# Kernel tuning notes

Measured on AMD Instinct MI355X. Metric: run time of the kernel, lower is better.

The kernel has to match this reference:

```python
import jax, jax.numpy as jnp
import numpy as np

B, L, D, H, NE, M = 4, 1024, 768, 12, 42, 8
OFFSET = 1
NEG = -1e9

def setup_inputs() -> dict:
    key = jax.random.key(0)
    k1, k2, k3, k4 = jax.random.split(key, 4)
    sequence_output = jax.random.normal(k1, (B, L, D), dtype=jnp.float32)
    attention = jax.random.uniform(k2, (B, H, L, L), dtype=jnp.float32)
    mention_idx = jax.random.randint(k3, (B, NE, M), 0, L - 2).astype(jnp.int32)
    mention_mask = jax.random.randint(k4, (B, NE, M), 0, 2).astype(jnp.int32)
    mention_mask = mention_mask.at[:, :, 0].set(1)  # every entity has >=1 mention
    return {"sequence_output": sequence_output, "attention": attention,
            "mention_idx": mention_idx, "mention_mask": mention_mask}

def reference(sequence_output, attention, mention_idx, mention_mask):
    b, l, d = sequence_output.shape
    h = attention.shape[1]
    idx = mention_idx + OFFSET                      # start + offset
    valid = (mention_mask > 0) & (idx < l)          # [B,NE,M], mirrors start+offset < c check
    idx = jnp.where(valid, idx, 0)

    # --- get_hrt: entity embedding = logsumexp over mentions, entity attn = mean over mentions ---
    flat = idx.reshape(b, -1)
    emb = jax.vmap(lambda s, i: s[i])(sequence_output, flat).reshape(b, NE, M, d)
    masked = jnp.where(valid[..., None], emb, NEG)
    ent_emb = jax.nn.logsumexp(masked, axis=2)      # [B,NE,D] (unused downstream, kept faithful)

    att = jax.vmap(lambda a, i: a[:, i])(attention, flat)        # [B,H,NE*M,L]
    att = att.reshape(b, h, NE, M, l)
    vmask = valid.astype(att.dtype)[:, None, :, :, None]         # [B,1,NE,M,1]
    cnt = jnp.maximum(valid.sum(axis=2), 1).astype(att.dtype)    # [B,NE]
    ent_att = (att * vmask).sum(axis=3) / cnt[:, None, :, None]  # [B,H,NE,L]

    # --- get_channel_map: ht_att = mean_h(h_att * t_att), row-normalize, contract with tokens ---
    ht_att = jnp.einsum('bhsl,bhtl->bstl', ent_att, ent_att) / h  # [B,NE,NE,L]
    ht_att = ht_att / (ht_att.sum(axis=-1, keepdims=True) + 1e-5)
    feature_map = jnp.einsum('bstl,bld->bstd', ht_att, sequence_output)  # [B,NE,NE,D]
    return feature_map
```

## Files before the change

kernel.cpp:

```cpp
#include <hip/hip_runtime.h>
#include <math.h>

#define B_    4
#define L_    1024
#define D_    768
#define H_    12
#define NE_   42
#define M_    8
#define NE2_  (NE_ * NE_)
#define NTRI_ 903
#define MPAD_ 1024
#define LC_   16
#define NCH_  (L_ / LC_)

typedef unsigned short u16;
typedef unsigned int   u32;
typedef __attribute__((ext_vector_type(2))) float f32x2;

__device__ __forceinline__ u16 f2bf(float f) {
    union { float f; u32 u; } c; c.f = f;
    u32 u = c.u;
    u32 r = (u + 0x7FFFu + ((u >> 16) & 1u)) >> 16;
    return (u16)r;
}

__global__ __launch_bounds__(128) void ent_att_kernel(
    const float* __restrict__ att, const int* __restrict__ midx,
    const int* __restrict__ mmask, float* __restrict__ ent) {
    const int h = blockIdx.x, e = blockIdx.y, b = blockIdx.z;
    const int t  = threadIdx.x;
    const int l0 = t * 8;
    const int mb = (b * NE_ + e) * M_;
    const size_t abase = ((size_t)(b * H_ + h)) * L_ * L_;

    float acc[8] = {0.f,0.f,0.f,0.f,0.f,0.f,0.f,0.f};
    int cnt = 0;
    for (int m = 0; m < M_; ++m) {
        int  im = midx[mb + m] + 1;
        bool v  = (mmask[mb + m] > 0) && (im < L_);
        if (v) {
            ++cnt;
            const float* row = att + abase + (size_t)im * L_ + l0;
            float4 x0 = *(const float4*)(row);
            float4 x1 = *(const float4*)(row + 4);
            acc[0] += x0.x; acc[1] += x0.y; acc[2] += x0.z; acc[3] += x0.w;
            acc[4] += x1.x; acc[5] += x1.y; acc[6] += x1.z; acc[7] += x1.w;
        }
    }
    const float s = 1.0f / (float)(cnt < 1 ? 1 : cnt);
    float* o = ent + (((size_t)(b * H_ + h)) * NE_ + e) * L_ + l0;
    *(float4*)(o)     = make_float4(acc[0]*s, acc[1]*s, acc[2]*s, acc[3]*s);
    *(float4*)(o + 4) = make_float4(acc[4]*s, acc[5]*s, acc[6]*s, acc[7]*s);
}

__global__ __launch_bounds__(256) void transpose_kernel(
    const float* __restrict__ S, u16* __restrict__ T) {
    __shared__ u16 tile[32][33];
    const int b  = blockIdx.z;
    const int n0 = blockIdx.x * 32;
    const int k0 = blockIdx.y * 32;
    const int tx = threadIdx.x, ty = threadIdx.y;
    const float* Sb = S + (size_t)b * L_ * D_;
    u16*         Tb = T + (size_t)b * D_ * L_;
    #pragma unroll
    for (int i = 0; i < 4; ++i)
        tile[ty + i*8][tx] = f2bf(Sb[(size_t)(k0 + ty + i*8) * D_ + (n0 + tx)]);
    __syncthreads();
    #pragma unroll
    for (int i = 0; i < 4; ++i)
        Tb[(size_t)(n0 + ty + i*8) * L_ + (k0 + tx)] = tile[tx][ty + i*8];
}

__global__ __launch_bounds__(256) void gram_kernel(
    const float* __restrict__ ent,
    u16* __restrict__ W,
    float* __restrict__ psum)
{
    __shared__ float E[H_ * NE_ * 18 + 8];
    const int gid   = blockIdx.x;
    const int xcd   = gid & 7, rr = gid >> 3;
    const int chunk = xcd * 8 + (rr & 7);
    const int b     = rr >> 3;
    const int l0    = chunk * LC_;
    const int tid   = threadIdx.x;

    const float* Eb = ent + (size_t)b * (H_ * NE_) * L_ + l0;
    for (int i = tid; i < H_ * NE_ * 4; i += 256) {
        const int row = i >> 2, sub = (i & 3) * 4;
        float4 v = *(const float4*)(Eb + (size_t)row * L_ + sub);
        f32x2* d = (f32x2*)&E[row * 18 + sub];
        d[0] = f32x2{v.x, v.y};
        d[1] = f32x2{v.z, v.w};
    }
    __syncthreads();

    if (tid < 231) {
        const int st = tid % 21, tt = tid / 21;
        const int s0 = 2 * st, t0 = 4 * tt;
        if (s0 <= t0 + 3) {
            const int e2 = (t0 + 2 < NE_) ? t0 + 2 : NE_ - 1;
            const int e3 = (t0 + 3 < NE_) ? t0 + 3 : NE_ - 1;
            float ps[2][4] = {};
            for (int l2 = 0; l2 < LC_ / 2; ++l2) {
                const int ll = 2 * l2;
                f32x2 c[2][4] = {};
                #pragma unroll
                for (int h = 0; h < H_; ++h) {
                    const float* Eh = E + h * (NE_ * 18);
                    f32x2 a0 = *(const f32x2*)&Eh[(s0    ) * 18 + ll];
                    f32x2 a1 = *(const f32x2*)&Eh[(s0 + 1) * 18 + ll];
                    f32x2 b0 = *(const f32x2*)&Eh[(t0    ) * 18 + ll];
                    f32x2 b1 = *(const f32x2*)&Eh[(t0 + 1) * 18 + ll];
                    f32x2 b2 = *(const f32x2*)&Eh[(e2    ) * 18 + ll];
                    f32x2 b3 = *(const f32x2*)&Eh[(e3    ) * 18 + ll];
                    c[0][0] += a0 * b0; c[0][1] += a0 * b1;
                    c[0][2] += a0 * b2; c[0][3] += a0 * b3;
                    c[1][0] += a1 * b0; c[1][1] += a1 * b1;
                    c[1][2] += a1 * b2; c[1][3] += a1 * b3;
                }
                #pragma unroll
                for (int si = 0; si < 2; ++si) {
                    #pragma unroll
                    for (int tj = 0; tj < 4; ++tj) {
                        const int s = s0 + si, t = t0 + tj;
                        if (t < NE_ && s <= t) {
                            const int q = (s * (85 - s)) / 2 + (t - s);
                            u32 w = (u32)f2bf(c[si][tj][0]) |
                                    ((u32)f2bf(c[si][tj][1]) << 16);
                            *(u32*)(W + ((size_t)b * MPAD_ + q) * L_ + l0 + ll) = w;
                            ps[si][tj] += c[si][tj][0] + c[si][tj][1];
                        }
                    }
                }
            }
            #pragma unroll
            for (int si = 0; si < 2; ++si)
                #pragma unroll
                for (int tj = 0; tj < 4; ++tj) {
                    const int s = s0 + si, t = t0 + tj;
                    if (t < NE_ && s <= t) {
                        const int q = (s * (85 - s)) / 2 + (t - s);
                        psum[((size_t)b * MPAD_ + q) * NCH_ + chunk] = ps[si][tj];
                    }
                }
        }
    } else {
        for (int q = NTRI_ + (tid - 231); q < MPAD_; q += 25) {
            u16* wr = W + ((size_t)b * MPAD_ + q) * L_ + l0;
            uint4 z; z.x = z.y = z.z = z.w = 0u;
            *(uint4*)(wr)     = z;
            *(uint4*)(wr + 8) = z;
        }
    }
}

__global__ __launch_bounds__(256) void rscale_kernel(
    const float* __restrict__ psum, float* __restrict__ rscale) {
    const int g = blockIdx.x * 256 + threadIdx.x;
    if (g >= B_ * NTRI_) return;
    const int b = g / NTRI_, q = g % NTRI_;
    const float* p = psum + ((size_t)b * MPAD_ + q) * NCH_;
    float s = 0.f;
    #pragma unroll
    for (int i = 0; i < NCH_; ++i) s += p[i];
    rscale[b * MPAD_ + q] = 1.0f / (s + (float)H_ * 1e-5f);
}

typedef __attribute__((ext_vector_type(8))) __bf16 bf16x8;
typedef __attribute__((ext_vector_type(4))) float  f32x4;

__global__ __launch_bounds__(256) void gemm_kernel(
    const u16* __restrict__ W, const u16* __restrict__ T,
    const float* __restrict__ rscale, float* __restrict__ out) {
    __shared__ __align__(16) u16 As[128 * 32];
    __shared__ __align__(16) u16 Bs[128 * 32];
    const int b = blockIdx.z;
    const u16* Ab = W + (size_t)b * MPAD_ * L_ + (size_t)blockIdx.x * 128 * L_;
    const u16* Bb = T + (size_t)b * D_   * L_ + (size_t)blockIdx.y * 128 * L_;
    const int tid  = threadIdx.x;
    const int wave = tid >> 6, lane = tid & 63;
    const int wm = (wave & 1) * 64, wn = (wave >> 1) * 64;
    const int rm = lane & 15, kq = (lane >> 4) * 8;

    f32x4 acc[4][4] = {};

    for (int k0 = 0; k0 < L_; k0 += 32) {
        __syncthreads();
        #pragma unroll
        for (int i = 0; i < 2; ++i) {
            int c = i * 256 + tid;
            int row = c >> 2, ko = (c & 3) * 8;
            __builtin_amdgcn_global_load_lds(
                (const __attribute__((address_space(1))) void*)(Ab + (size_t)row * L_ + k0 + ko),
                (__attribute__((address_space(3))) void*)(&As[c * 8]), 16, 0, 0);
            __builtin_amdgcn_global_load_lds(
                (const __attribute__((address_space(1))) void*)(Bb + (size_t)row * L_ + k0 + ko),
                (__attribute__((address_space(3))) void*)(&Bs[c * 8]), 16, 0, 0);
        }
        __syncthreads();

        bf16x8 af[4], bfr[4];
        #pragma unroll
        for (int i = 0; i < 4; ++i)
            af[i]  = *(const bf16x8*)&As[(wm + i*16 + rm) * 32 + kq];
        #pragma unroll
        for (int j = 0; j < 4; ++j)
            bfr[j] = *(const bf16x8*)&Bs[(wn + j*16 + rm) * 32 + kq];
        #pragma unroll
        for (int i = 0; i < 4; ++i)
            #pragma unroll
            for (int j = 0; j < 4; ++j)
                acc[i][j] = __builtin_amdgcn_mfma_f32_16x16x32_bf16(
                                af[i], bfr[j], acc[i][j], 0, 0, 0);
    }

    const int row0 = blockIdx.x * 128 + wm;
    const int col0 = blockIdx.y * 128 + wn;
    const int cl = lane & 15, rq = (lane >> 4) * 4;
    float* Ob = out + (size_t)b * NE2_ * D_;
    const float* rsb = rscale + (size_t)b * MPAD_;
    #pragma unroll
    for (int i = 0; i < 4; ++i) {
        #pragma unroll
        for (int r = 0; r < 4; ++r) {
            const int q = row0 + i*16 + rq + r;
            if (q < NTRI_) {
                int s = (int)(42.5f - sqrtf(1806.25f - 2.0f * (float)q));
                if (s < 0) s = 0; if (s > 41) s = 41;
                int base = (s * (85 - s)) >> 1;
                if (q < base) { --s; base = (s * (85 - s)) >> 1; }
                else { const int nb = ((s + 1) * (84 - s)) >> 1;
                       if (q >= nb) { ++s; base = nb; } }
                const int t = s + (q - base);
                const float sc = rsb[q];
                float* O1 = Ob + (size_t)(s * NE_ + t) * D_ + col0 + cl;
                float* O2 = Ob + (size_t)(t * NE_ + s) * D_ + col0 + cl;
                #pragma unroll
                for (int j = 0; j < 4; ++j) {
                    const float v = acc[i][j][r] * sc;
                    O1[j * 16] = v;
                    O2[j * 16] = v;
                }
            }
        }
    }
}

#define ENT_BYTES  (8257536)
#define W_BYTES    (8388608)
#define ST_BYTES   (6291456)
#define PSUM_BYTES (1048576)

extern "C" void kernel_launch(void* const* d_in, const int* in_sizes, int n_in,
                              void* d_out, int out_size, void* d_ws, size_t ws_size,
                              hipStream_t stream) {
    const float* seq   = (const float*)d_in[0];
    const float* att   = (const float*)d_in[1];
    const int*   midx  = (const int*)d_in[2];
    const int*   mmask = (const int*)d_in[3];
    float* out = (float*)d_out;

    char* ws  = (char*)d_ws;
    float* ent    = (float*)ws;
    u16*   W      = (u16*)(ws + ENT_BYTES);
    u16*   ST     = (u16*)(ws + ENT_BYTES + W_BYTES);
    float* psum   = (float*)(ws + ENT_BYTES + W_BYTES + ST_BYTES);
    float* rscale = (float*)(ws + ENT_BYTES + W_BYTES + ST_BYTES + PSUM_BYTES);

    ent_att_kernel<<<dim3(H_, NE_, B_), 128, 0, stream>>>(att, midx, mmask, ent);
    transpose_kernel<<<dim3(D_/32, L_/32, B_), dim3(32, 8), 0, stream>>>(seq, ST);
    gram_kernel<<<256, 256, 0, stream>>>(ent, W, psum);
    rscale_kernel<<<(B_ * NTRI_ + 255) / 256, 256, 0, stream>>>(psum, rscale);
    gemm_kernel<<<dim3(MPAD_/128, D_/128, B_), 256, 0, stream>>>(W, ST, rscale, out);
}
```

Baseline: 299.3 us.

## Merge prep kernels, fold rscale into GEMM, double-buffer swizzled LDS tiles

Combines the entity-attention and transpose kernels into one launch and computes the row-normalisation reciprocals inside the GEMM prologue, which removes a separate kernel. The GEMM now uses K=64 tiles that are double-buffered in LDS with an XOR swizzle, so global-to-LDS loads of the next tile overlap the MFMA work on the current one and LDS bank conflicts are reduced. This removes two launch boundaries and cuts per-iteration synchronisation. In exchange the GEMM uses four times the LDS per block, which can lower occupancy.

Measured after the change: 294.1 us. No clear change (-1.7%).

```diff
diff --git a/kernel.cpp b/kernel.cpp
--- a/kernel.cpp
+++ b/kernel.cpp
@@ -24,51 +24,56 @@
     return (u16)r;
 }
 
-__global__ __launch_bounds__(128) void ent_att_kernel(
+#define TBLKS (D_/32 * L_/32 * B_)
+#define EBLKS (H_ * NE_ * B_)
+
+__global__ __launch_bounds__(256) void prep_kernel(
+    const float* __restrict__ S, u16* __restrict__ T,
     const float* __restrict__ att, const int* __restrict__ midx,
     const int* __restrict__ mmask, float* __restrict__ ent) {
-    const int h = blockIdx.x, e = blockIdx.y, b = blockIdx.z;
-    const int t  = threadIdx.x;
-    const int l0 = t * 8;
-    const int mb = (b * NE_ + e) * M_;
-    const size_t abase = ((size_t)(b * H_ + h)) * L_ * L_;
-
-    float acc[8] = {0.f,0.f,0.f,0.f,0.f,0.f,0.f,0.f};
-    int cnt = 0;
-    for (int m = 0; m < M_; ++m) {
-        int  im = midx[mb + m] + 1;
-        bool v  = (mmask[mb + m] > 0) && (im < L_);
-        if (v) {
-            ++cnt;
-            const float* row = att + abase + (size_t)im * L_ + l0;
-            float4 x0 = *(const float4*)(row);
-            float4 x1 = *(const float4*)(row + 4);
-            acc[0] += x0.x; acc[1] += x0.y; acc[2] += x0.z; acc[3] += x0.w;
-            acc[4] += x1.x; acc[5] += x1.y; acc[6] += x1.z; acc[7] += x1.w;
-        }
-    }
-    const float s = 1.0f / (float)(cnt < 1 ? 1 : cnt);
-    float* o = ent + (((size_t)(b * H_ + h)) * NE_ + e) * L_ + l0;
-    *(float4*)(o)     = make_float4(acc[0]*s, acc[1]*s, acc[2]*s, acc[3]*s);
-    *(float4*)(o + 4) = make_float4(acc[4]*s, acc[5]*s, acc[6]*s, acc[7]*s);
-}
-
-__global__ __launch_bounds__(256) void transpose_kernel(
-    const float* __restrict__ S, u16* __restrict__ T) {
-    __shared__ u16 tile[32][33];
-    const int b  = blockIdx.z;
-    const int n0 = blockIdx.x * 32;
-    const int k0 = blockIdx.y * 32;
-    const int tx = threadIdx.x, ty = threadIdx.y;
-    const float* Sb = S + (size_t)b * L_ * D_;
-    u16*         Tb = T + (size_t)b * D_ * L_;
-    #pragma unroll
-    for (int i = 0; i < 4; ++i)
-        tile[ty + i*8][tx] = f2bf(Sb[(size_t)(k0 + ty + i*8) * D_ + (n0 + tx)]);
-    __syncthreads();
-    #pragma unroll
-    for (int i = 0; i < 4; ++i)
-        Tb[(size_t)(n0 + ty + i*8) * L_ + (k0 + tx)] = tile[tx][ty + i*8];
+    const int bid = blockIdx.x;
+    const int tid = threadIdx.x;
+
+    if (bid < TBLKS) {
+        __shared__ u16 tile[32][33];
+        const int bx = bid % (D_/32);
+        const int by = (bid / (D_/32)) % (L_/32);
+        const int b  = bid / (D_/32 * L_/32);
+        const int n0 = bx * 32, k0 = by * 32;
+        const int tx = tid & 31, ty = tid >> 5;
+        const float* Sb = S + (size_t)b * L_ * D_;
+        u16*         Tb = T + (size_t)b * D_ * L_;
+        #pragma unroll
+        for (int i = 0; i < 4; ++i)
+            tile[ty + i*8][tx] = f2bf(Sb[(size_t)(k0 + ty + i*8) * D_ + (n0 + tx)]);
+        __syncthreads();
+        #pragma unroll
+        for (int i = 0; i < 4; ++i)
+            Tb[(size_t)(n0 + ty + i*8) * L_ + (k0 + tx)] = tile[tx][ty + i*8];
+    } else {
+        const int eb = bid - TBLKS;
+        const int h  = eb % H_;
+        const int e  = (eb / H_) % NE_;
+        const int b  = eb / (H_ * NE_);
+        const int l0 = tid * 4;
+        const int mb = (b * NE_ + e) * M_;
+        const size_t abase = ((size_t)(b * H_ + h)) * L_ * L_;
+
+        float a0 = 0.f, a1 = 0.f, a2 = 0.f, a3 = 0.f;
+        int cnt = 0;
+        for (int m = 0; m < M_; ++m) {
+            int  im = midx[mb + m] + 1;
+            bool v  = (mmask[mb + m] > 0) && (im < L_);
+            if (v) {
+                ++cnt;
+                float4 x = *(const float4*)(att + abase + (size_t)im * L_ + l0);
+                a0 += x.x; a1 += x.y; a2 += x.z; a3 += x.w;
+            }
+        }
+        const float s = 1.0f / (float)(cnt < 1 ? 1 : cnt);
+        float* o = ent + (((size_t)(b * H_ + h)) * NE_ + e) * L_ + l0;
+        *(float4*)(o) = make_float4(a0*s, a1*s, a2*s, a3*s);
+    }
 }
 
 __global__ __launch_bounds__(256) void gram_kernel(
@@ -154,26 +159,15 @@
     }
 }
 
-__global__ __launch_bounds__(256) void rscale_kernel(
-    const float* __restrict__ psum, float* __restrict__ rscale) {
-    const int g = blockIdx.x * 256 + threadIdx.x;
-    if (g >= B_ * NTRI_) return;
-    const int b = g / NTRI_, q = g % NTRI_;
-    const float* p = psum + ((size_t)b * MPAD_ + q) * NCH_;
-    float s = 0.f;
-    #pragma unroll
-    for (int i = 0; i < NCH_; ++i) s += p[i];
-    rscale[b * MPAD_ + q] = 1.0f / (s + (float)H_ * 1e-5f);
-}
-
 typedef __attribute__((ext_vector_type(8))) __bf16 bf16x8;
 typedef __attribute__((ext_vector_type(4))) float  f32x4;
 
 __global__ __launch_bounds__(256) void gemm_kernel(
     const u16* __restrict__ W, const u16* __restrict__ T,
-    const float* __restrict__ rscale, float* __restrict__ out) {
-    __shared__ __align__(16) u16 As[128 * 32];
-    __shared__ __align__(16) u16 Bs[128 * 32];
+    const float* __restrict__ psum, float* __restrict__ out) {
+    __shared__ __align__(16) u16 As[2][128 * 64];
+    __shared__ __align__(16) u16 Bs[2][128 * 64];
+    __shared__ float rs_s[128];
     const int b = blockIdx.z;
     const u16* Ab = W + (size_t)b * MPAD_ * L_ + (size_t)blockIdx.x * 128 * L_;
     const u16* Bb = T + (size_t)b * D_   * L_ + (size_t)blockIdx.y * 128 * L_;
@@ -182,43 +176,71 @@
     const int wm = (wave & 1) * 64, wn = (wave >> 1) * 64;
     const int rm = lane & 15, kq = (lane >> 4) * 8;
 
-    f32x4 acc[4][4] = {};
-
-    for (int k0 = 0; k0 < L_; k0 += 32) {
-        __syncthreads();
-        #pragma unroll
-        for (int i = 0; i < 2; ++i) {
-            int c = i * 256 + tid;
-            int row = c >> 2, ko = (c & 3) * 8;
+    auto STAGE = [&](int buf, int k0) {
+        #pragma unroll
+        for (int i = 0; i < 4; ++i) {
+            const int c   = i * 256 + tid;
+            const int row = c >> 3, cp = c & 7;
+            const int ko  = ((cp ^ (row & 7)) << 3);
             __builtin_amdgcn_global_load_lds(
                 (const __attribute__((address_space(1))) void*)(Ab + (size_t)row * L_ + k0 + ko),
-                (__attribute__((address_space(3))) void*)(&As[c * 8]), 16, 0, 0);
+                (__attribute__((address_space(3))) void*)(&As[buf][c * 8]), 16, 0, 0);
             __builtin_amdgcn_global_load_lds(
                 (const __attribute__((address_space(1))) void*)(Bb + (size_t)row * L_ + k0 + ko),
-                (__attribute__((address_space(3))) void*)(&Bs[c * 8]), 16, 0, 0);
-        }
-        __syncthreads();
-
-        bf16x8 af[4], bfr[4];
-        #pragma unroll
-        for (int i = 0; i < 4; ++i)
-            af[i]  = *(const bf16x8*)&As[(wm + i*16 + rm) * 32 + kq];
-        #pragma unroll
-        for (int j = 0; j < 4; ++j)
-            bfr[j] = *(const bf16x8*)&Bs[(wn + j*16 + rm) * 32 + kq];
-        #pragma unroll
-        for (int i = 0; i < 4; ++i)
-            #pragma unroll
-            for (int j = 0; j < 4; ++j)
-                acc[i][j] = __builtin_amdgcn_mfma_f32_16x16x32_bf16(
-                                af[i], bfr[j], acc[i][j], 0, 0, 0);
+                (__attribute__((address_space(3))) void*)(&Bs[buf][c * 8]), 16, 0, 0);
+        }
+    };
+
+    f32x4 acc[4][4] = {};
+
+    STAGE(0, 0);
+    if (tid < 128) {
+        const float* p = psum + ((size_t)b * MPAD_ + (size_t)blockIdx.x * 128 + tid) * NCH_;
+        float s = 0.f;
+        #pragma unroll
+        for (int i = 0; i < NCH_ / 4; ++i) {
+            float4 v = *(const float4*)(p + 4 * i);
+            s += v.x + v.y + v.z + v.w;
+        }
+        rs_s[tid] = 1.0f / (s + (float)H_ * 1e-5f);
+    }
+    asm volatile("s_waitcnt vmcnt(0) lgkmcnt(0)" ::: "memory");
+    __builtin_amdgcn_s_barrier();
+
+    int cur = 0;
+    for (int kt = 0; kt < 16; ++kt) {
+        if (kt < 15) STAGE(cur ^ 1, (kt + 1) * 64);
+
+        #pragma unroll
+        for (int kk = 0; kk < 64; kk += 32) {
+            bf16x8 af[4], bfr[4];
+            #pragma unroll
+            for (int i = 0; i < 4; ++i) {
+                const int ra = wm + i*16 + rm;
+                af[i]  = *(const bf16x8*)&As[cur][ra * 64 + ((((kk + kq) >> 3) ^ (ra & 7)) << 3)];
+            }
+            #pragma unroll
+            for (int j = 0; j < 4; ++j) {
+                const int rb = wn + j*16 + rm;
+                bfr[j] = *(const bf16x8*)&Bs[cur][rb * 64 + ((((kk + kq) >> 3) ^ (rb & 7)) << 3)];
+            }
+            #pragma unroll
+            for (int i = 0; i < 4; ++i)
+                #pragma unroll
+                for (int j = 0; j < 4; ++j)
+                    acc[i][j] = __builtin_amdgcn_mfma_f32_16x16x32_bf16(
+                                    af[i], bfr[j], acc[i][j], 0, 0, 0);
+        }
+
+        asm volatile("s_waitcnt vmcnt(0)" ::: "memory");
+        __builtin_amdgcn_s_barrier();
+        cur ^= 1;
     }
 
     const int row0 = blockIdx.x * 128 + wm;
     const int col0 = blockIdx.y * 128 + wn;
     const int cl = lane & 15, rq = (lane >> 4) * 4;
     float* Ob = out + (size_t)b * NE2_ * D_;
-    const float* rsb = rscale + (size_t)b * MPAD_;
     #pragma unroll
     for (int i = 0; i < 4; ++i) {
         #pragma unroll
@@ -232,7 +254,7 @@
                 else { const int nb = ((s + 1) * (84 - s)) >> 1;
                        if (q >= nb) { ++s; base = nb; } }
                 const int t = s + (q - base);
-                const float sc = rsb[q];
+                const float sc = rs_s[q - blockIdx.x * 128];
                 float* O1 = Ob + (size_t)(s * NE_ + t) * D_ + col0 + cl;
                 float* O2 = Ob + (size_t)(t * NE_ + s) * D_ + col0 + cl;
                 #pragma unroll
@@ -249,7 +271,6 @@
 #define ENT_BYTES  (8257536)
 #define W_BYTES    (8388608)
 #define ST_BYTES   (6291456)
-#define PSUM_BYTES (1048576)
 
 extern "C" void kernel_launch(void* const* d_in, const int* in_sizes, int n_in,
                               void* d_out, int out_size, void* d_ws, size_t ws_size,
@@ -261,15 +282,12 @@
     float* out = (float*)d_out;
 
     char* ws  = (char*)d_ws;
-    float* ent    = (float*)ws;
-    u16*   W      = (u16*)(ws + ENT_BYTES);
-    u16*   ST     = (u16*)(ws + ENT_BYTES + W_BYTES);
-    float* psum   = (float*)(ws + ENT_BYTES + W_BYTES + ST_BYTES);
-    float* rscale = (float*)(ws + ENT_BYTES + W_BYTES + ST_BYTES + PSUM_BYTES);
-
-    ent_att_kernel<<<dim3(H_, NE_, B_), 128, 0, stream>>>(att, midx, mmask, ent);
-    transpose_kernel<<<dim3(D_/32, L_/32, B_), dim3(32, 8), 0, stream>>>(seq, ST);
-    gram_kernel<<<256, 256, 0, stream>>>(ent, W, psum);
-    rscale_kernel<<<(B_ * NTRI_ + 255) / 256, 256, 0, stream>>>(psum, rscale);
-    gemm_kernel<<<dim3(MPAD_/128, D_/128, B_), 256, 0, stream>>>(W, ST, rscale, out);
-}
+    float* ent  = (float*)ws;
+    u16*   Wb   = (u16*)(ws + ENT_BYTES);
+    u16*   ST   = (u16*)(ws + ENT_BYTES + W_BYTES);
+    float* psum = (float*)(ws + ENT_BYTES + W_BYTES + ST_BYTES);
+
+    prep_kernel<<<TBLKS + EBLKS, 256, 0, stream>>>(seq, ST, att, midx, mmask, ent);
+    gram_kernel<<<256, 256, 0, stream>>>(ent, Wb, psum);
+    gemm_kernel<<<dim3(MPAD_/128, D_/128, B_), 256, 0, stream>>>(Wb, ST, psum, out);
+}
```
